# Kernel optimization log

Measured on AMD Instinct MI355X. Metric: run time of the kernel, lower is better.

The kernel has to match this reference:

```python
import jax, jax.numpy as jnp
import numpy as np

B, N, E = 4, 10000, 160000
IN, OUT, H, ED = 64, 128, 2, 1
SLOPE = 0.2  # GATv2Conv default negative_slope


def _seg_softmax(logits, seg, n):
    # logits: [Ef, H]; softmax over edges sharing the same dst node, per head
    m = jax.ops.segment_max(logits, seg, num_segments=n)
    e = jnp.exp(logits - m[seg])
    d = jax.ops.segment_sum(e, seg, num_segments=n)
    return e / d[seg]


def setup_inputs() -> dict:
    key = jax.random.key(0)
    ks = jax.random.split(key, 10)
    s = 0.05
    return {
        "node_feats": jax.random.normal(ks[0], (B, N, IN), jnp.float32),
        "edge_index": jax.random.randint(ks[1], (2, E), 0, N, dtype=jnp.int64),
        "edge_attr": jax.random.normal(ks[2], (E, ED), jnp.float32),
        "Wl": jax.random.normal(ks[3], (IN, H * OUT), jnp.float32) * s,
        "bl": jax.random.normal(ks[4], (H * OUT,), jnp.float32) * s,
        "Wr": jax.random.normal(ks[5], (IN, H * OUT), jnp.float32) * s,
        "br": jax.random.normal(ks[6], (H * OUT,), jnp.float32) * s,
        "We": jax.random.normal(ks[7], (ED, H * OUT), jnp.float32) * s,
        "att": jax.random.normal(ks[8], (H, OUT), jnp.float32) * s,
        "bias": jax.random.normal(ks[9], (H * OUT,), jnp.float32) * s,
    }


def reference(node_feats, edge_index, edge_attr, Wl, bl, Wr, br, We, att, bias):
    src, dst = edge_index[0], edge_index[1]
    # PyG add_self_loops(fill_value='mean'): self-loop attr = mean of incoming edge attrs per node
    ones = jnp.ones((E,), edge_attr.dtype)
    deg = jax.ops.segment_sum(ones, dst, num_segments=N)
    loop_attr = jax.ops.segment_sum(edge_attr, dst, num_segments=N) / jnp.maximum(deg, 1.0)[:, None]
    sl = jnp.arange(N)
    src_f = jnp.concatenate([src, sl])           # [Ef] with Ef = E + N
    dst_f = jnp.concatenate([dst, sl])
    e_feat = (jnp.concatenate([edge_attr, loop_attr], axis=0) @ We).reshape(-1, H, OUT)  # [Ef,H,C]

    xl = (node_feats @ Wl + bl).reshape(B, N, H, OUT)  # lin_l(x)
    xr = (node_feats @ Wr + br).reshape(B, N, H, OUT)  # lin_r(x)

    # GATv2: score on leaky_relu(x_l[src] + x_r[dst] + lin_edge(e))
    msg = jax.nn.leaky_relu(xl[:, src_f] + xr[:, dst_f] + e_feat[None], SLOPE)  # [B,Ef,H,C]
    logits = jnp.einsum('behc,hc->beh', msg, att)                               # [B,Ef,H]
    alpha = jax.vmap(lambda l: _seg_softmax(l, dst_f, N))(logits)               # [B,Ef,H]

    weighted = alpha[..., None] * xl[:, src_f]                                  # [B,Ef,H,C]
    out = jax.vmap(lambda w: jax.ops.segment_sum(w, dst_f, num_segments=N))(weighted)  # [B,N,H,C]
    return out.reshape(B, N, H * OUT) + bias
```

## Files before the change

kernel.cpp:

```cpp
#include <hip/hip_runtime.h>
#include <hip/hip_bf16.h>

#define BQ 4
#define NN 10000
#define EE 160000
#define HC 256
#define SLOPEK 0.2f
#define CAPE 128

typedef __attribute__((ext_vector_type(8))) short bf16x8;
typedef __attribute__((ext_vector_type(4))) float f32x4;

__device__ __forceinline__ unsigned short f2bf(float f) {
    unsigned int u = __float_as_uint(f);
    u = (u + 0x7FFFu + ((u >> 16) & 1u)) >> 16;
    return (unsigned short)u;
}
__device__ __forceinline__ float bflo(unsigned int u) { return __uint_as_float(u << 16); }
__device__ __forceinline__ float bfhi(unsigned int u) { return __uint_as_float(u & 0xFFFF0000u); }

__global__ __launch_bounds__(256) void k_wpack(
    const float* __restrict__ Wl, const float* __restrict__ bl,
    const float* __restrict__ Wr, const float* __restrict__ br,
    unsigned short* __restrict__ wp, float* __restrict__ bp)
{
    const int tid = blockIdx.x * 256 + threadIdx.x;
    if (tid < 32768) {
        const int j  = tid & 7;
        const int l  = (tid >> 3) & 63;
        const int s  = (tid >> 9) & 1;
        const int ct = tid >> 10;
        const int col = ct * 16 + (l & 15);
        const int kk  = s * 32 + ((l >> 4) << 3) + j;
        const float w = (col < 256) ? Wl[kk * 256 + col] : Wr[kk * 256 + (col - 256)];
        wp[tid] = f2bf(w);
    } else if (tid < 32768 + 512) {
        const int c = tid - 32768;
        bp[c] = (c < 256) ? bl[c] : br[c - 256];
    }
}

__global__ __launch_bounds__(256) void k_pre(
    const float* __restrict__ x, const unsigned short* __restrict__ wp,
    const float* __restrict__ bp,
    unsigned short* __restrict__ xl, unsigned short* __restrict__ xr,
    const int* __restrict__ ei, const float* __restrict__ ea,
    int* __restrict__ cnt, float* __restrict__ asum,
    int2* __restrict__ cmeta)
{
    if (blockIdx.x >= 625) {
        const int e = (blockIdx.x - 625) * 256 + threadIdx.x;
        const int   sn = ei[e];
        const int   d  = ei[EE + e];
        const float a  = ea[e];
        const int pos  = atomicAdd(&cnt[d], 1);
        atomicAdd(&asum[d], a);
        if (pos < CAPE - 1)
            cmeta[d * CAPE + pos] = make_int2(sn << 10, __float_as_int(a));
        return;
    }
    const int w = threadIdx.x >> 6, l = threadIdx.x & 63;
    const int row0 = blockIdx.x * 64 + w * 16;
    const int arow = row0 + (l & 15);
    const float* xp = x + (size_t)arow * 64 + ((l >> 4) << 3);

    bf16x8 a[2];
#pragma unroll
    for (int s = 0; s < 2; ++s) {
        const float4 lo = *reinterpret_cast<const float4*>(xp + s * 32);
        const float4 hi = *reinterpret_cast<const float4*>(xp + s * 32 + 4);
        union { bf16x8 v; unsigned short u[8]; } t;
        t.u[0] = f2bf(lo.x); t.u[1] = f2bf(lo.y); t.u[2] = f2bf(lo.z); t.u[3] = f2bf(lo.w);
        t.u[4] = f2bf(hi.x); t.u[5] = f2bf(hi.y); t.u[6] = f2bf(hi.z); t.u[7] = f2bf(hi.w);
        a[s] = t.v;
    }
    const int colb = l & 15;
    const int rsub = (l >> 4) << 2;

    for (int g = 0; g < 8; ++g) {
        f32x4 acc[4] = {{0.f,0.f,0.f,0.f},{0.f,0.f,0.f,0.f},
                        {0.f,0.f,0.f,0.f},{0.f,0.f,0.f,0.f}};
#pragma unroll
        for (int c = 0; c < 4; ++c) {
            const int ct = g * 4 + c;
            const bf16x8 b0 = *reinterpret_cast<const bf16x8*>(wp + (((ct * 2 + 0) * 64 + l) << 3));
            const bf16x8 b1 = *reinterpret_cast<const bf16x8*>(wp + (((ct * 2 + 1) * 64 + l) << 3));
            acc[c] = __builtin_amdgcn_mfma_f32_16x16x32_bf16(a[0], b0, acc[c], 0, 0, 0);
            acc[c] = __builtin_amdgcn_mfma_f32_16x16x32_bf16(a[1], b1, acc[c], 0, 0, 0);
        }
#pragma unroll
        for (int c = 0; c < 4; ++c) {
            const int col = (g * 4 + c) * 16 + colb;
            const float bv = bp[col];
#pragma unroll
            for (int r = 0; r < 4; ++r) {
                const int row = row0 + rsub + r;
                const int bb = (row >= 20000) ? (row >= 30000 ? 3 : 2)
                                              : (row >= 10000 ? 1 : 0);
                const int n = row - bb * NN;
                const unsigned short h = f2bf(acc[c][r] + bv);
                if (col < 256) xl[(((size_t)(n * 4 + bb)) << 8) + col] = h;
                else           xr[(((size_t)(n * 4 + bb)) << 8) + (col - 256)] = h;
            }
        }
    }
}

__global__ __launch_bounds__(256) void k_gat(
    const unsigned short* __restrict__ xl, const unsigned short* __restrict__ xr,
    const int* __restrict__ cnt, const float* __restrict__ asum,
    const int2* __restrict__ cmeta,
    const float* __restrict__ We, const float* __restrict__ att,
    const float* __restrict__ bias, float* __restrict__ outp)
{
    const int t  = threadIdx.x;
    const int wv = t >> 6, ln = t & 63;
    const int n  = blockIdx.x * 4 + wv;
    const int c  = ln & 15;
    const int b  = ln >> 4;
    const int ch0 = c << 4;

    int dg0 = cnt[n];
    if (dg0 > 63) dg0 = 63;
    const int dg = __builtin_amdgcn_readfirstlane(dg0);
    const int2 md0 = cmeta[n * CAPE + ln];
    int   ms = md0.x;
    float ma = __int_as_float(md0.y);
    if (ln == dg) {
        ms = n << 10;
        ma = asum[n] / fmaxf((float)dg, 1.0f);
    }
    const int ntot = dg + 1;

    float we16[16], at16[16], xr16[16], acc[16];
    {
        const float4* Wp = reinterpret_cast<const float4*>(We + ch0);
        const float4* Ap = reinterpret_cast<const float4*>(att + ch0);
#pragma unroll
        for (int j = 0; j < 4; ++j) {
            const float4 w4 = Wp[j], a4 = Ap[j];
            we16[4*j+0] = w4.x; we16[4*j+1] = w4.y; we16[4*j+2] = w4.z; we16[4*j+3] = w4.w;
            at16[4*j+0] = a4.x; at16[4*j+1] = a4.y; at16[4*j+2] = a4.z; at16[4*j+3] = a4.w;
        }
        const uint4* Xp = reinterpret_cast<const uint4*>(
            xr + ((size_t)n << 10) + (b << 8) + ch0);
        const uint4 r0 = Xp[0], r1 = Xp[1];
        xr16[0]=bflo(r0.x); xr16[1]=bfhi(r0.x); xr16[2]=bflo(r0.y); xr16[3]=bfhi(r0.y);
        xr16[4]=bflo(r0.z); xr16[5]=bfhi(r0.z); xr16[6]=bflo(r0.w); xr16[7]=bfhi(r0.w);
        xr16[8]=bflo(r1.x); xr16[9]=bfhi(r1.x); xr16[10]=bflo(r1.y); xr16[11]=bfhi(r1.y);
        xr16[12]=bflo(r1.z); xr16[13]=bfhi(r1.z); xr16[14]=bflo(r1.w); xr16[15]=bfhi(r1.w);
    }
#pragma unroll
    for (int k = 0; k < 16; ++k) acc[k] = 0.f;
    float sh = 0.f;

    const unsigned short* __restrict__ xlp = xl + (b << 8) + ch0;

    uint4 A0, B0, A1, B1, A2, B2, A3, B3;
    float ea0, ea1, ea2, ea3;

#define LOADSLOT(S, IDX) do { \
        const int ii_ = (IDX); \
        const int ic_ = ii_ < dg ? ii_ : dg; \
        const int   s_ = __builtin_amdgcn_readlane(ms, ic_); \
        ea##S = __int_as_float(__builtin_amdgcn_readlane(__float_as_int(ma), ic_)); \
        const unsigned short* p_ = xlp + s_; \
        A##S = *reinterpret_cast<const uint4*>(p_); \
        B##S = *reinterpret_cast<const uint4*>(p_ + 8); \
    } while (0)

    auto edgeC = [&](const uint4& A, const uint4& Bv, float a0) {
        float xv[16];
        xv[0]=bflo(A.x);  xv[1]=bfhi(A.x);  xv[2]=bflo(A.y);  xv[3]=bfhi(A.y);
        xv[4]=bflo(A.z);  xv[5]=bfhi(A.z);  xv[6]=bflo(A.w);  xv[7]=bfhi(A.w);
        xv[8]=bflo(Bv.x); xv[9]=bfhi(Bv.x); xv[10]=bflo(Bv.y); xv[11]=bfhi(Bv.y);
        xv[12]=bflo(Bv.z); xv[13]=bfhi(Bv.z); xv[14]=bflo(Bv.w); xv[15]=bfhi(Bv.w);

        float q[4];
#pragma unroll
        for (int g = 0; g < 4; ++g) {
            float v = fmaf(a0, we16[4*g], xv[4*g] + xr16[4*g]);
            v = fmaf(SLOPEK - 1.f, fminf(v, 0.f), v);
            float qq = v * at16[4*g];
#pragma unroll
            for (int k = 1; k < 4; ++k) {
                float u = fmaf(a0, we16[4*g+k], xv[4*g+k] + xr16[4*g+k]);
                u = fmaf(SLOPEK - 1.f, fminf(u, 0.f), u);
                qq = fmaf(u, at16[4*g+k], qq);
            }
            q[g] = qq;
        }
        float p = (q[0] + q[1]) + (q[2] + q[3]);
        p += __shfl_xor(p, 1);
        p += __shfl_xor(p, 2);
        p += __shfl_xor(p, 4);
        const float e = __expf(p);
        sh += e;
#pragma unroll
        for (int k = 0; k < 16; ++k) acc[k] = fmaf(e, xv[k], acc[k]);
    };

    LOADSLOT(0, 0);
    LOADSLOT(1, 1);
    LOADSLOT(2, 2);

    int i = 0;
    for (; i + 3 < ntot; i += 4) {
        LOADSLOT(3, i + 3); edgeC(A0, B0, ea0);
        LOADSLOT(0, i + 4); edgeC(A1, B1, ea1);
        LOADSLOT(1, i + 5); edgeC(A2, B2, ea2);
        LOADSLOT(2, i + 6); edgeC(A3, B3, ea3);
    }
    if (i     < ntot) edgeC(A0, B0, ea0);
    if (i + 1 < ntot) edgeC(A1, B1, ea1);
    if (i + 2 < ntot) edgeC(A2, B2, ea2);
#undef LOADSLOT

    const float inv = 1.0f / sh;
    float* ob = outp + (((size_t)(b * NN + n)) << 8) + ch0;
    const float4* Bp = reinterpret_cast<const float4*>(bias + ch0);
#pragma unroll
    for (int j = 0; j < 4; ++j) {
        const float4 b4 = Bp[j];
        float4 o;
        o.x = fmaf(acc[4*j+0], inv, b4.x);
        o.y = fmaf(acc[4*j+1], inv, b4.y);
        o.z = fmaf(acc[4*j+2], inv, b4.z);
        o.w = fmaf(acc[4*j+3], inv, b4.w);
        reinterpret_cast<float4*>(ob)[j] = o;
    }
}

extern "C" void kernel_launch(void* const* d_in, const int* in_sizes, int n_in,
                              void* d_out, int out_size, void* d_ws, size_t ws_size,
                              hipStream_t stream)
{
    (void)in_sizes; (void)n_in; (void)out_size; (void)ws_size;
    const float* x    = (const float*)d_in[0];
    const int*   ei   = (const int*)d_in[1];
    const float* ea   = (const float*)d_in[2];
    const float* Wl   = (const float*)d_in[3];
    const float* bl   = (const float*)d_in[4];
    const float* Wr   = (const float*)d_in[5];
    const float* br   = (const float*)d_in[6];
    const float* We   = (const float*)d_in[7];
    const float* att  = (const float*)d_in[8];
    const float* bias = (const float*)d_in[9];
    float* outp = (float*)d_out;

    const size_t R = (size_t)BQ * NN;
    unsigned short* xl16 = (unsigned short*)d_ws;
    unsigned short* xr16 = xl16 + R * HC;
    int*   cnt   = (int*)(xr16 + R * HC);
    float* asum  = (float*)(cnt + NN);
    int2*  cmeta = (int2*)(asum + NN);
    unsigned short* wp = (unsigned short*)(cmeta + (size_t)NN * CAPE);
    float* bp    = (float*)(wp + 32768);

    hipMemsetAsync(cnt, 0, sizeof(int) * NN * 2, stream);

    k_wpack<<<130, 256, 0, stream>>>(Wl, bl, Wr, br, wp, bp);
    k_pre  <<<1250, 256, 0, stream>>>(x, wp, bp, xl16, xr16,
                                      ei, ea, cnt, asum, cmeta);
    k_gat  <<<NN / 4, 256, 0, stream>>>(xl16, xr16, cnt, asum, cmeta,
                                        We, att, bias, outp);
}
```

Measured before the change: 95.81 us.

## Use packed f32x2 math and persistent single-wave blocks in GAT kernel

The GAT aggregation kernel now runs one wave per block with a grid-stride loop over nodes, so each block handles about three nodes and loads the We/att constants once. The per-edge score and accumulation math is rewritten on two-wide float vectors so the compiler can emit packed FP32 FMA/min instructions, roughly halving VALU instruction count. The trade-off is fewer, longer-lived blocks, which may cause load imbalance across nodes of varying degree.

```diff
diff --git a/kernel.cpp b/kernel.cpp
--- a/kernel.cpp
+++ b/kernel.cpp
@@ -7,9 +7,11 @@
 #define HC 256
 #define SLOPEK 0.2f
 #define CAPE 128
+#define GATBLK 3334
 
 typedef __attribute__((ext_vector_type(8))) short bf16x8;
 typedef __attribute__((ext_vector_type(4))) float f32x4;
+typedef __attribute__((ext_vector_type(2))) float f32x2;
 
 __device__ __forceinline__ unsigned short f2bf(float f) {
     unsigned int u = __float_as_uint(f);
@@ -18,6 +20,9 @@
 }
 __device__ __forceinline__ float bflo(unsigned int u) { return __uint_as_float(u << 16); }
 __device__ __forceinline__ float bfhi(unsigned int u) { return __uint_as_float(u & 0xFFFF0000u); }
+__device__ __forceinline__ f32x2 bf2(unsigned int u) {
+    return (f32x2){__uint_as_float(u << 16), __uint_as_float(u & 0xFFFF0000u)};
+}
 
 __global__ __launch_bounds__(256) void k_wpack(
     const float* __restrict__ Wl, const float* __restrict__ bl,
@@ -106,58 +111,63 @@
     }
 }
 
-__global__ __launch_bounds__(256) void k_gat(
+__global__ __launch_bounds__(64, 4) void k_gat(
     const unsigned short* __restrict__ xl, const unsigned short* __restrict__ xr,
     const int* __restrict__ cnt, const float* __restrict__ asum,
     const int2* __restrict__ cmeta,
     const float* __restrict__ We, const float* __restrict__ att,
     const float* __restrict__ bias, float* __restrict__ outp)
 {
-    const int t  = threadIdx.x;
-    const int wv = t >> 6, ln = t & 63;
-    const int n  = blockIdx.x * 4 + wv;
+    const int ln = threadIdx.x;
     const int c  = ln & 15;
     const int b  = ln >> 4;
     const int ch0 = c << 4;
 
-    int dg0 = cnt[n];
-    if (dg0 > 63) dg0 = 63;
-    const int dg = __builtin_amdgcn_readfirstlane(dg0);
-    const int2 md0 = cmeta[n * CAPE + ln];
-    int   ms = md0.x;
-    float ma = __int_as_float(md0.y);
-    if (ln == dg) {
-        ms = n << 10;
-        ma = asum[n] / fmaxf((float)dg, 1.0f);
-    }
-    const int ntot = dg + 1;
-
-    float we16[16], at16[16], xr16[16], acc[16];
+    f32x2 we2[8], at2[8];
     {
         const float4* Wp = reinterpret_cast<const float4*>(We + ch0);
         const float4* Ap = reinterpret_cast<const float4*>(att + ch0);
 #pragma unroll
         for (int j = 0; j < 4; ++j) {
             const float4 w4 = Wp[j], a4 = Ap[j];
-            we16[4*j+0] = w4.x; we16[4*j+1] = w4.y; we16[4*j+2] = w4.z; we16[4*j+3] = w4.w;
-            at16[4*j+0] = a4.x; at16[4*j+1] = a4.y; at16[4*j+2] = a4.z; at16[4*j+3] = a4.w;
-        }
-        const uint4* Xp = reinterpret_cast<const uint4*>(
-            xr + ((size_t)n << 10) + (b << 8) + ch0);
-        const uint4 r0 = Xp[0], r1 = Xp[1];
-        xr16[0]=bflo(r0.x); xr16[1]=bfhi(r0.x); xr16[2]=bflo(r0.y); xr16[3]=bfhi(r0.y);
-        xr16[4]=bflo(r0.z); xr16[5]=bfhi(r0.z); xr16[6]=bflo(r0.w); xr16[7]=bfhi(r0.w);
-        xr16[8]=bflo(r1.x); xr16[9]=bfhi(r1.x); xr16[10]=bflo(r1.y); xr16[11]=bfhi(r1.y);
-        xr16[12]=bflo(r1.z); xr16[13]=bfhi(r1.z); xr16[14]=bflo(r1.w); xr16[15]=bfhi(r1.w);
-    }
-#pragma unroll
-    for (int k = 0; k < 16; ++k) acc[k] = 0.f;
-    float sh = 0.f;
-
-    const unsigned short* __restrict__ xlp = xl + (b << 8) + ch0;
-
-    uint4 A0, B0, A1, B1, A2, B2, A3, B3;
-    float ea0, ea1, ea2, ea3;
+            we2[2*j+0] = (f32x2){w4.x, w4.y};
+            we2[2*j+1] = (f32x2){w4.z, w4.w};
+            at2[2*j+0] = (f32x2){a4.x, a4.y};
+            at2[2*j+1] = (f32x2){a4.z, a4.w};
+        }
+    }
+    const f32x2 km1 = {SLOPEK - 1.f, SLOPEK - 1.f};
+    const f32x2 z2  = {0.f, 0.f};
+
+    for (int n = blockIdx.x; n < NN; n += GATBLK) {
+        int dg0 = cnt[n];
+        if (dg0 > 63) dg0 = 63;
+        const int dg = __builtin_amdgcn_readfirstlane(dg0);
+        const int2 md0 = cmeta[n * CAPE + ln];
+        int   ms = md0.x;
+        float ma = __int_as_float(md0.y);
+        if (ln == dg) {
+            ms = n << 10;
+            ma = asum[n] / fmaxf((float)dg, 1.0f);
+        }
+        const int ntot = dg + 1;
+
+        f32x2 xr2[8], acc2[8];
+        {
+            const uint4* Xp = reinterpret_cast<const uint4*>(
+                xr + ((size_t)n << 10) + (b << 8) + ch0);
+            const uint4 r0 = Xp[0], r1 = Xp[1];
+            xr2[0] = bf2(r0.x); xr2[1] = bf2(r0.y); xr2[2] = bf2(r0.z); xr2[3] = bf2(r0.w);
+            xr2[4] = bf2(r1.x); xr2[5] = bf2(r1.y); xr2[6] = bf2(r1.z); xr2[7] = bf2(r1.w);
+        }
+#pragma unroll
+        for (int k = 0; k < 8; ++k) acc2[k] = z2;
+        float sh = 0.f;
+
+        const unsigned short* __restrict__ xlp = xl + (b << 8) + ch0;
+
+        uint4 A0, B0, A1, B1, A2, B2, A3, B3;
+        float ea0, ea1, ea2, ea3;
 
 #define LOADSLOT(S, IDX) do { \
         const int ii_ = (IDX); \
@@ -169,65 +179,64 @@
         B##S = *reinterpret_cast<const uint4*>(p_ + 8); \
     } while (0)
 
-    auto edgeC = [&](const uint4& A, const uint4& Bv, float a0) {
-        float xv[16];
-        xv[0]=bflo(A.x);  xv[1]=bfhi(A.x);  xv[2]=bflo(A.y);  xv[3]=bfhi(A.y);
-        xv[4]=bflo(A.z);  xv[5]=bfhi(A.z);  xv[6]=bflo(A.w);  xv[7]=bfhi(A.w);
-        xv[8]=bflo(Bv.x); xv[9]=bfhi(Bv.x); xv[10]=bflo(Bv.y); xv[11]=bfhi(Bv.y);
-        xv[12]=bflo(Bv.z); xv[13]=bfhi(Bv.z); xv[14]=bflo(Bv.w); xv[15]=bfhi(Bv.w);
-
-        float q[4];
-#pragma unroll
-        for (int g = 0; g < 4; ++g) {
-            float v = fmaf(a0, we16[4*g], xv[4*g] + xr16[4*g]);
-            v = fmaf(SLOPEK - 1.f, fminf(v, 0.f), v);
-            float qq = v * at16[4*g];
-#pragma unroll
-            for (int k = 1; k < 4; ++k) {
-                float u = fmaf(a0, we16[4*g+k], xv[4*g+k] + xr16[4*g+k]);
-                u = fmaf(SLOPEK - 1.f, fminf(u, 0.f), u);
-                qq = fmaf(u, at16[4*g+k], qq);
+        auto edgeC = [&](const uint4& A, const uint4& Bv, float a0) {
+            f32x2 xv2[8];
+            xv2[0] = bf2(A.x);  xv2[1] = bf2(A.y);  xv2[2] = bf2(A.z);  xv2[3] = bf2(A.w);
+            xv2[4] = bf2(Bv.x); xv2[5] = bf2(Bv.y); xv2[6] = bf2(Bv.z); xv2[7] = bf2(Bv.w);
+
+            const f32x2 a02 = {a0, a0};
+            f32x2 qa = z2, qb = z2;
+#pragma unroll
+            for (int j = 0; j < 8; ++j) {
+                f32x2 s = xv2[j] + xr2[j];
+                f32x2 v = __builtin_elementwise_fma(a02, we2[j], s);
+                f32x2 vm = __builtin_elementwise_min(v, z2);
+                v = __builtin_elementwise_fma(km1, vm, v);
+                if (j & 1) qb = __builtin_elementwise_fma(v, at2[j], qb);
+                else       qa = __builtin_elementwise_fma(v, at2[j], qa);
             }
-            q[g] = qq;
-        }
-        float p = (q[0] + q[1]) + (q[2] + q[3]);
-        p += __shfl_xor(p, 1);
-        p += __shfl_xor(p, 2);
-        p += __shfl_xor(p, 4);
-        const float e = __expf(p);
-        sh += e;
-#pragma unroll
-        for (int k = 0; k < 16; ++k) acc[k] = fmaf(e, xv[k], acc[k]);
-    };
-
-    LOADSLOT(0, 0);
-    LOADSLOT(1, 1);
-    LOADSLOT(2, 2);
-
-    int i = 0;
-    for (; i + 3 < ntot; i += 4) {
-        LOADSLOT(3, i + 3); edgeC(A0, B0, ea0);
-        LOADSLOT(0, i + 4); edgeC(A1, B1, ea1);
-        LOADSLOT(1, i + 5); edgeC(A2, B2, ea2);
-        LOADSLOT(2, i + 6); edgeC(A3, B3, ea3);
-    }
-    if (i     < ntot) edgeC(A0, B0, ea0);
-    if (i + 1 < ntot) edgeC(A1, B1, ea1);
-    if (i + 2 < ntot) edgeC(A2, B2, ea2);
+            const f32x2 q2 = qa + qb;
+            float p = q2.x + q2.y;
+            p += __shfl_xor(p, 1);
+            p += __shfl_xor(p, 2);
+            p += __shfl_xor(p, 4);
+            const float e = __expf(p);
+            sh += e;
+            const f32x2 e2 = {e, e};
+#pragma unroll
+            for (int j = 0; j < 8; ++j)
+                acc2[j] = __builtin_elementwise_fma(e2, xv2[j], acc2[j]);
+        };
+
+        LOADSLOT(0, 0);
+        LOADSLOT(1, 1);
+        LOADSLOT(2, 2);
+
+        int i = 0;
+        for (; i + 3 < ntot; i += 4) {
+            LOADSLOT(3, i + 3); edgeC(A0, B0, ea0);
+            LOADSLOT(0, i + 4); edgeC(A1, B1, ea1);
+            LOADSLOT(1, i + 5); edgeC(A2, B2, ea2);
+            LOADSLOT(2, i + 6); edgeC(A3, B3, ea3);
+        }
+        if (i     < ntot) edgeC(A0, B0, ea0);
+        if (i + 1 < ntot) edgeC(A1, B1, ea1);
+        if (i + 2 < ntot) edgeC(A2, B2, ea2);
 #undef LOADSLOT
 
-    const float inv = 1.0f / sh;
-    float* ob = outp + (((size_t)(b * NN + n)) << 8) + ch0;
-    const float4* Bp = reinterpret_cast<const float4*>(bias + ch0);
-#pragma unroll
-    for (int j = 0; j < 4; ++j) {
-        const float4 b4 = Bp[j];
-        float4 o;
-        o.x = fmaf(acc[4*j+0], inv, b4.x);
-        o.y = fmaf(acc[4*j+1], inv, b4.y);
-        o.z = fmaf(acc[4*j+2], inv, b4.z);
-        o.w = fmaf(acc[4*j+3], inv, b4.w);
-        reinterpret_cast<float4*>(ob)[j] = o;
+        const float inv = 1.0f / sh;
+        float* ob = outp + (((size_t)(b * NN + n)) << 8) + ch0;
+        const float4* Bp = reinterpret_cast<const float4*>(bias + ch0);
+#pragma unroll
+        for (int j = 0; j < 4; ++j) {
+            const float4 b4 = Bp[j];
+            float4 o;
+            o.x = fmaf(acc2[2*j+0].x, inv, b4.x);
+            o.y = fmaf(acc2[2*j+0].y, inv, b4.y);
+            o.z = fmaf(acc2[2*j+1].x, inv, b4.z);
+            o.w = fmaf(acc2[2*j+1].y, inv, b4.w);
+            reinterpret_cast<float4*>(ob)[j] = o;
+        }
     }
 }
 
@@ -262,6 +271,6 @@
     k_wpack<<<130, 256, 0, stream>>>(Wl, bl, Wr, br, wp, bp);
     k_pre  <<<1250, 256, 0, stream>>>(x, wp, bp, xl16, xr16,
                                       ei, ea, cnt, asum, cmeta);
-    k_gat  <<<NN / 4, 256, 0, stream>>>(xl16, xr16, cnt, asum, cmeta,
-                                        We, att, bias, outp);
-}
+    k_gat  <<<GATBLK, 64, 0, stream>>>(xl16, xr16, cnt, asum, cmeta,
+                                       We, att, bias, outp);
+}
```

Result: slower. 110.3 us (+15.1%).
